# Performance work log

Hardware: AMD Instinct MI355X
Metric: run time of the kernel (lower is better)

The kernel has to match this reference:

```python
import jax, jax.numpy as jnp
import numpy as np


def _edt_background(gt):
    """Exact Euclidean distance transform of (1 - gt): distance from each pixel
    to the nearest foreground (gt==1) pixel. gt: [H, W] int. Returns [H, W] f32.
    Separable formulation: g(i,j) = 1D distance along row i to nearest fg;
    D(i,j)^2 = min_{i'} ( (i-i')^2 + g(i',j)^2 ), which is the exact 2D EDT.
    """
    H, W = gt.shape
    BIG = jnp.float32(H + W)  # upper bound on any true distance
    fg = gt > 0
    col = jnp.arange(W, dtype=jnp.float32)
    # nearest fg index to the left (running max of fg column index)
    left = jax.lax.cummax(jnp.where(fg, col, -BIG), axis=1)
    d_left = col[None, :] - left
    # nearest fg index to the right: running max of (-col) from the right = -min(col)
    right = jax.lax.cummax(jnp.where(fg, -col, -BIG)[:, ::-1], axis=1)[:, ::-1]
    d_right = (-right) - col[None, :]
    g = jnp.clip(jnp.minimum(d_left, d_right), 0.0, BIG)  # [H, W] 1D row distances
    g2 = g * g
    row = jnp.arange(H, dtype=jnp.float32)
    di2 = (row[:, None] - row[None, :]) ** 2              # [H, H]
    d2 = jnp.min(di2[:, :, None] + g2[None, :, :], axis=1)  # [H, W]
    return jnp.sqrt(d2)


def setup_inputs() -> dict:
    key = jax.random.key(0)
    k1, k2 = jax.random.split(key)
    B, H, W = 16, 384, 384
    logits = jax.random.normal(k1, (B, 1, H, W), dtype=jnp.float32)
    targets = jax.random.randint(k2, (B, 1, H, W), 0, 2).astype(jnp.int32)
    return {"logits": logits, "targets": targets}


def reference(logits, targets):
    probs = jax.nn.sigmoid(logits)            # [B,1,H,W]
    gt = targets[:, 0]                        # [B,H,W] int
    # sequential map over batch keeps the [H,H,W] EDT intermediate per-sample
    dist = jax.lax.map(_edt_background, gt)   # [B,H,W] f32
    tgt_f = gt.astype(jnp.float32)
    per_sample = jnp.mean(jnp.abs(probs[:, 0] - tgt_f) * dist, axis=(1, 2))
    return jnp.mean(per_sample)
```

## Files before the change

kernel.cpp:

```cpp
#include <hip/hip_runtime.h>
#include <math.h>


#define BB 16
#define HH 384
#define WW 384
#define WPR 12
#define WPRP 13
#define SW 16
#define NBLK (WW / SW)
#define RPB (HH / NBLK)
#define THREADS 512
#define NBLOCKS (BB * NBLK)
#define BIGD 768
#define WORDS_PER_IMG (HH * WPR)
#define WPB (RPB * WPR)
#define PART_BASE (BB * WORDS_PER_IMG)
#define MAGA 0x9E3779B9u
#define TAG64 (((unsigned long long)MAGA) << 32)

__global__ __launch_bounds__(THREADS, 2) void boundary_fused(
    const float* __restrict__ logits, const int* __restrict__ gt,
    unsigned long long* ws, float* __restrict__ out) {
  const int p = blockIdx.x;
  const int xcd = p & 7;
  const int slot = p >> 3;
  const int sub = (slot >= NBLK) ? 1 : 0;
  const int b = xcd * 2 + sub;
  const int st = slot - sub * NBLK;
  const int j0 = st * SW;
  const int r0 = st * RPB;
  const float* __restrict__ lg = logits + b * HH * WW;
  const int* __restrict__ gimg = gt + b * HH * WW;
  unsigned long long* mimg = ws + (size_t)b * WORDS_PER_IMG;

  __shared__ unsigned m_s[HH * WPRP];
  __shared__ unsigned short g_s[HH * SW];
  __shared__ float red[THREADS / 64];

  float4 xf[3];
#pragma unroll
  for (int t = 0; t < 3; ++t) {
    const int s = threadIdx.x + t * THREADS;
    const int i = s >> 2;
    const int jj = (s & 3) * 4;
    xf[t] = *(const float4*)(lg + i * WW + j0 + jj);
  }

  if (threadIdx.x < WPB) {
    const int q = threadIdx.x;
    const int rr = q / WPR;
    const int w = q - rr * WPR;
    const int r = r0 + rr;
    const int4* __restrict__ g4 = (const int4*)(gimg + r * WW + w * 32);
    unsigned word = 0;
#pragma unroll
    for (int k = 0; k < 8; ++k) {
      const int4 v = g4[k];
      word |= ((unsigned)(v.x != 0)) << (k * 4);
      word |= ((unsigned)(v.y != 0)) << (k * 4 + 1);
      word |= ((unsigned)(v.z != 0)) << (k * 4 + 2);
      word |= ((unsigned)(v.w != 0)) << (k * 4 + 3);
    }
    atomicExch(mimg + (r * WPR + w), TAG64 | (unsigned long long)word);
  }

#pragma unroll
  for (int t = 0; t < 9; ++t) {
    const int wi = threadIdx.x + t * THREADS;
    unsigned long long v =
        __hip_atomic_load(mimg + wi, __ATOMIC_RELAXED, __HIP_MEMORY_SCOPE_AGENT);
    while ((unsigned)(v >> 32) != MAGA) {
      __builtin_amdgcn_s_sleep(2);
      v = __hip_atomic_load(mimg + wi, __ATOMIC_RELAXED, __HIP_MEMORY_SCOPE_AGENT);
    }
    const int row = wi / WPR;
    const int w = wi - row * WPR;
    m_s[row * WPRP + w] = (unsigned)v;
  }
  __syncthreads();

#pragma unroll
  for (int t = 0; t < 3; ++t) {
    const int s = threadIdx.x + t * THREADS;
    const int i = s >> 2;
    const int jj = (s & 3) * 4;
    const int j = j0 + jj;
    const unsigned* __restrict__ mr = m_s + i * WPRP;
    const int w = j >> 5;
    const int bpos = j & 31;
    const unsigned cur = mr[w];

    int jL = -0x40000;
    if ((cur & (0xFFFFFFFFu >> (31 - bpos))) == 0u) {
      for (int ww = w - 1; ww >= 0; --ww) {
        const unsigned x = mr[ww];
        if (x) { jL = ww * 32 + 31 - __clz(x); break; }
      }
    }
    int jR = 0x40000;
    if ((cur & (0xFFFFFFFFu << (bpos + 3))) == 0u) {
      for (int ww = w + 1; ww < WPR; ++ww) {
        const unsigned x = mr[ww];
        if (x) { jR = ww * 32 + __ffs(x) - 1; break; }
      }
    }
    unsigned short g4[4];
#pragma unroll
    for (int c = 0; c < 4; ++c) {
      const int bc = bpos + c;
      const int jc = j + c;
      const unsigned lm = cur & (0xFFFFFFFFu >> (31 - bc));
      const unsigned rm = cur & (0xFFFFFFFFu << bc);
      const int dl = lm ? (bc - (31 - __clz(lm))) : (jc - jL);
      const int dr = rm ? ((__ffs(rm) - 1) - bc) : (jR - jc);
      g4[c] = (unsigned short)min(min(dl, dr), BIGD);
    }
    ushort4 gv; gv.x = g4[0]; gv.y = g4[1]; gv.z = g4[2]; gv.w = g4[3];
    *(ushort4*)(g_s + i * SW + jj) = gv;
  }
  __syncthreads();

  float acc = 0.0f;
#pragma unroll
  for (int t = 0; t < 3; ++t) {
    const int s = threadIdx.x + t * THREADS;
    const int i = s >> 2;
    const int jj = (s & 3) * 4;
    const ushort4 gv = *(const ushort4*)(g_s + i * SW + jj);
    const float4 x4 = xf[t];
    const int gg[4] = {gv.x, gv.y, gv.z, gv.w};
    const float xs[4] = {x4.x, x4.y, x4.z, x4.w};
#pragma unroll
    for (int c = 0; c < 4; ++c) {
      int best = gg[c] * gg[c];
      for (int r = 1; r * r < best; ++r) {
        const int im = i - r, ip = i + r;
        if (im >= 0) { const int v = g_s[im * SW + jj + c]; best = min(best, r * r + v * v); }
        if (ip < HH) { const int v = g_s[ip * SW + jj + c]; best = min(best, r * r + v * v); }
      }
      const float dist = __builtin_amdgcn_sqrtf((float)best);
      const float p2 = __builtin_amdgcn_rcpf(1.0f + __expf(-xs[c]));
      acc += p2 * dist;
    }
  }

  for (int off = 32; off > 0; off >>= 1) acc += __shfl_down(acc, off, 64);
  const int lane = threadIdx.x & 63;
  const int wid = threadIdx.x >> 6;
  if (lane == 0) red[wid] = acc;
  __syncthreads();
  if (threadIdx.x == 0) {
    float ssum = 0.0f;
    for (int w = 0; w < THREADS / 64; ++w) ssum += red[w];
    atomicExch(ws + PART_BASE + p,
               TAG64 | (unsigned long long)__float_as_uint(ssum));
  }

  if (p == 0) {
    const int t = threadIdx.x;
    float v = 0.0f;
    if (t < NBLOCKS) {
      unsigned long long a = __hip_atomic_load(ws + PART_BASE + t,
                                               __ATOMIC_RELAXED,
                                               __HIP_MEMORY_SCOPE_AGENT);
      while ((unsigned)(a >> 32) != MAGA) {
        __builtin_amdgcn_s_sleep(2);
        a = __hip_atomic_load(ws + PART_BASE + t, __ATOMIC_RELAXED,
                              __HIP_MEMORY_SCOPE_AGENT);
      }
      v = __uint_as_float((unsigned)a);
    }
    for (int off = 32; off > 0; off >>= 1) v += __shfl_down(v, off, 64);
    __syncthreads();
    if (lane == 0) red[wid] = v;
    __syncthreads();
    if (t == 0) {
      float s = 0.0f;
      for (int w = 0; w < THREADS / 64; ++w) s += red[w];
      out[0] = s * (1.0f / (float)(BB * HH * WW));
    }
  }
}

extern "C" void kernel_launch(void* const* d_in, const int* in_sizes, int n_in,
                              void* d_out, int out_size, void* d_ws, size_t ws_size,
                              hipStream_t stream) {
  const float* logits = (const float*)d_in[0];
  const int* targets = (const int*)d_in[1];
  float* out = (float*)d_out;
  unsigned long long* ws = (unsigned long long*)d_ws;

  boundary_fused<<<NBLOCKS, THREADS, 0, stream>>>(logits, targets, ws, out);
}
```

Baseline: 79.51 us.

## Replace per-word tagged mask exchange with per-block flags and hierarchical reduction

Mask words are now written as plain 32-bit stores followed by a threadfence and one tagged flag per block, instead of a 64-bit tagged atomic per word. Consumers poll only the 24 producer flags for their image, then bulk-load the packed mask pairs, which halves traffic and removes per-word spin loops. The final reduction becomes two-level: each image's st==0 block sums its 24 partials, and block 0 sums the 16 image sums, which avoids one block serially polling 384 slots. It relies on fence ordering for correctness across blocks, and stale flags in a reused workspace remain a risk.

Measured after the change: 154.0 us. 93.7% more time.

```diff
diff --git a/kernel.cpp b/kernel.cpp
--- a/kernel.cpp
+++ b/kernel.cpp
@@ -14,10 +14,27 @@
 #define NBLOCKS (BB * NBLK)
 #define BIGD 768
 #define WORDS_PER_IMG (HH * WPR)
+#define PAIRS_PER_IMG (WORDS_PER_IMG / 2)
 #define WPB (RPB * WPR)
-#define PART_BASE (BB * WORDS_PER_IMG)
+#define FLAG_BASE ((BB * WORDS_PER_IMG) / 2)
+#define PART_BASE (FLAG_BASE + NBLOCKS)
+#define ISUM_BASE (PART_BASE + NBLOCKS)
 #define MAGA 0x9E3779B9u
 #define TAG64 (((unsigned long long)MAGA) << 32)
+
+__device__ __forceinline__ int blk_of(int bb, int st) {
+  return (bb >> 1) + 8 * ((bb & 1) * NBLK + st);
+}
+
+__device__ __forceinline__ float poll_tagged(unsigned long long* slot) {
+  unsigned long long a =
+      __hip_atomic_load(slot, __ATOMIC_RELAXED, __HIP_MEMORY_SCOPE_AGENT);
+  while ((unsigned)(a >> 32) != MAGA) {
+    __builtin_amdgcn_s_sleep(2);
+    a = __hip_atomic_load(slot, __ATOMIC_RELAXED, __HIP_MEMORY_SCOPE_AGENT);
+  }
+  return __uint_as_float((unsigned)a);
+}
 
 __global__ __launch_bounds__(THREADS, 2) void boundary_fused(
     const float* __restrict__ logits, const int* __restrict__ gt,
@@ -32,7 +49,8 @@
   const int r0 = st * RPB;
   const float* __restrict__ lg = logits + b * HH * WW;
   const int* __restrict__ gimg = gt + b * HH * WW;
-  unsigned long long* mimg = ws + (size_t)b * WORDS_PER_IMG;
+  unsigned* mimg32 = (unsigned*)ws + b * WORDS_PER_IMG;
+  unsigned long long* mimg64 = ws + (size_t)b * PAIRS_PER_IMG;
 
   __shared__ unsigned m_s[HH * WPRP];
   __shared__ unsigned short g_s[HH * SW];
@@ -49,10 +67,7 @@
 
   if (threadIdx.x < WPB) {
     const int q = threadIdx.x;
-    const int rr = q / WPR;
-    const int w = q - rr * WPR;
-    const int r = r0 + rr;
-    const int4* __restrict__ g4 = (const int4*)(gimg + r * WW + w * 32);
+    const int4* __restrict__ g4 = (const int4*)(gimg + r0 * WW + q * 32);
     unsigned word = 0;
 #pragma unroll
     for (int k = 0; k < 8; ++k) {
@@ -62,21 +77,29 @@
       word |= ((unsigned)(v.z != 0)) << (k * 4 + 2);
       word |= ((unsigned)(v.w != 0)) << (k * 4 + 3);
     }
-    atomicExch(mimg + (r * WPR + w), TAG64 | (unsigned long long)word);
-  }
-
-#pragma unroll
-  for (int t = 0; t < 9; ++t) {
-    const int wi = threadIdx.x + t * THREADS;
-    unsigned long long v =
-        __hip_atomic_load(mimg + wi, __ATOMIC_RELAXED, __HIP_MEMORY_SCOPE_AGENT);
-    while ((unsigned)(v >> 32) != MAGA) {
-      __builtin_amdgcn_s_sleep(2);
-      v = __hip_atomic_load(mimg + wi, __ATOMIC_RELAXED, __HIP_MEMORY_SCOPE_AGENT);
-    }
-    const int row = wi / WPR;
-    const int w = wi - row * WPR;
-    m_s[row * WPRP + w] = (unsigned)v;
+    mimg32[r0 * WPR + q] = word;
+  }
+  __threadfence();
+  __syncthreads();
+  if (threadIdx.x == 0) {
+    atomicExch(ws + FLAG_BASE + p, TAG64 | 1ULL);
+  }
+
+  {
+    const int f = threadIdx.x & 31;
+    if (f < NBLK) (void)poll_tagged(ws + FLAG_BASE + blk_of(b, f));
+  }
+  __syncthreads();
+
+  for (int idx = threadIdx.x; idx < PAIRS_PER_IMG; idx += THREADS) {
+    const unsigned long long v =
+        __hip_atomic_load(mimg64 + idx, __ATOMIC_RELAXED, __HIP_MEMORY_SCOPE_AGENT);
+    const int wp = idx * 2;
+    const int row = wp / WPR;
+    const int w = wp - row * WPR;
+    unsigned* dst = m_s + row * WPRP + w;
+    dst[0] = (unsigned)v;
+    dst[1] = (unsigned)(v >> 32);
   }
   __syncthreads();
 
@@ -157,29 +180,21 @@
                TAG64 | (unsigned long long)__float_as_uint(ssum));
   }
 
-  if (p == 0) {
+  if (st == 0 && threadIdx.x < 64) {
     const int t = threadIdx.x;
-    float v = 0.0f;
-    if (t < NBLOCKS) {
-      unsigned long long a = __hip_atomic_load(ws + PART_BASE + t,
-                                               __ATOMIC_RELAXED,
-                                               __HIP_MEMORY_SCOPE_AGENT);
-      while ((unsigned)(a >> 32) != MAGA) {
-        __builtin_amdgcn_s_sleep(2);
-        a = __hip_atomic_load(ws + PART_BASE + t, __ATOMIC_RELAXED,
-                              __HIP_MEMORY_SCOPE_AGENT);
-      }
-      v = __uint_as_float((unsigned)a);
-    }
+    float v = (t < NBLK) ? poll_tagged(ws + PART_BASE + blk_of(b, t)) : 0.0f;
     for (int off = 32; off > 0; off >>= 1) v += __shfl_down(v, off, 64);
-    __syncthreads();
-    if (lane == 0) red[wid] = v;
-    __syncthreads();
     if (t == 0) {
-      float s = 0.0f;
-      for (int w = 0; w < THREADS / 64; ++w) s += red[w];
-      out[0] = s * (1.0f / (float)(BB * HH * WW));
-    }
+      atomicExch(ws + ISUM_BASE + b,
+                 TAG64 | (unsigned long long)__float_as_uint(v));
+    }
+  }
+
+  if (p == 0 && threadIdx.x < 64) {
+    const int t = threadIdx.x;
+    float v = (t < BB) ? poll_tagged(ws + ISUM_BASE + t) : 0.0f;
+    for (int off = 32; off > 0; off >>= 1) v += __shfl_down(v, off, 64);
+    if (t == 0) out[0] = v * (1.0f / (float)(BB * HH * WW));
   }
 }
 
```
